# Optimization experiments

Measured on AMD Instinct MI355X. Metric: run time of the kernel, lower is better.

Reference implementation:

```python
import jax, jax.numpy as jnp
import numpy as np

EPS = 1e-5

def _ln(x, s, b):
    mu = jnp.mean(x, axis=-1, keepdims=True)
    var = jnp.mean((x - mu) ** 2, axis=-1, keepdims=True)
    return (x - mu) * jax.lax.rsqrt(var + EPS) * s + b

def _gelu(x):
    return jax.nn.gelu(x, approximate=False)


def setup_inputs() -> dict:
    key = jax.random.key(0)
    ks = jax.random.split(key, 24)
    B, L, C, E, T, FC, MULT = 8, 4096, 128, 1048576, 512, 32, 2
    N = B * L
    inp = {}
    inp['feats'] = jax.random.normal(ks[0], (N, C), jnp.float32)
    inp['edge_index'] = jax.random.randint(ks[1], (2, E), 0, N, jnp.int32)
    inp['edge_attr'] = jax.random.normal(ks[2], (E, 2), jnp.float32) * 0.05  # relative coords
    inp['t'] = jax.random.normal(ks[3], (B, T), jnp.float32)
    inp['norm_vec'] = jnp.ones((N, 1), jnp.float32)
    # LayerNorms
    inp['ln1_scale'] = jnp.ones((C,), jnp.float32); inp['ln1_bias'] = jnp.zeros((C,), jnp.float32)
    inp['ln2_scale'] = jnp.ones((C,), jnp.float32); inp['ln2_bias'] = jnp.zeros((C,), jnp.float32)
    # time mlps: GELU -> Linear(T, 2C)
    sc = lambda k, sh: jax.random.normal(k, sh, jnp.float32) / np.sqrt(sh[0])
    inp['tmlp1_w'] = sc(ks[4], (T, 2 * C)); inp['tmlp1_b'] = jnp.zeros((2 * C,), jnp.float32)
    inp['tmlp2_w'] = sc(ks[5], (T, 2 * C)); inp['tmlp2_b'] = jnp.zeros((2 * C,), jnp.float32)
    # continuous-kernel MLP: 2 -> FC -> FC -> C (depthwise weights)
    inp['ker_w1'] = sc(ks[6], (2, FC)); inp['ker_b1'] = jnp.zeros((FC,), jnp.float32)
    inp['ker_w2'] = sc(ks[7], (FC, FC)); inp['ker_b2'] = jnp.zeros((FC,), jnp.float32)
    inp['ker_w3'] = sc(ks[8], (FC, C)); inp['ker_b3'] = jnp.zeros((C,), jnp.float32)
    inp['conv_bias'] = jnp.zeros((C,), jnp.float32)
    # feedforward mlp: C -> mult*C -> C
    inp['mlp_w1'] = sc(ks[9], (C, MULT * C)); inp['mlp_b1'] = jnp.zeros((MULT * C,), jnp.float32)
    inp['mlp_w2'] = sc(ks[10], (MULT * C, C)); inp['mlp_b2'] = jnp.zeros((C,), jnp.float32)
    return inp


def reference(feats, edge_index, edge_attr, t, norm_vec,
              ln1_scale, ln1_bias, ln2_scale, ln2_bias,
              tmlp1_w, tmlp1_b, tmlp2_w, tmlp2_b,
              ker_w1, ker_b1, ker_w2, ker_b2, ker_w3, ker_b3, conv_bias,
              mlp_w1, mlp_b1, mlp_w2, mlp_b2):
    N, C = feats.shape
    B = t.shape[0]
    q = N // B  # nodes per image

    def modulate(f, ln_s, ln_b, tw, tb):
        h = _ln(f, ln_s, ln_b)
        tm = _gelu(t) @ tw + tb                       # [B, 2C]
        tm = jnp.repeat(tm, q, axis=0)                # [(B q), 2C]
        scale, shift = jnp.split(tm, 2, axis=-1)
        return h * (1.0 + scale) + shift

    # pre-conv modulation
    h = modulate(feats, ln1_scale, ln1_bias, tmlp1_w, tmlp1_b)

    # continuous conv: per-edge depthwise kernel from edge_attr
    k = _gelu(edge_attr @ ker_w1 + ker_b1)
    k = _gelu(k @ ker_w2 + ker_b2)
    w = k @ ker_w3 + ker_b3                           # [E, C]
    src, dst = edge_index[0], edge_index[1]
    msg = w * h[src]                                  # gather + weight  [E, C]
    h = jax.ops.segment_sum(msg, dst, num_segments=N) + conv_bias
    h = h / norm_vec                                  # tg_div normalization

    x = feats + h                                     # residual 1

    # post-conv modulation + MLP
    h2 = modulate(x, ln2_scale, ln2_bias, tmlp2_w, tmlp2_b)
    h2 = _gelu(h2 @ mlp_w1 + mlp_b1) @ mlp_w2 + mlp_b2
    return x + h2                                     # residual 2
```

## Files before the change

### kernel.cpp

```cpp
#include <hip/hip_runtime.h>
#include <hip/hip_bf16.h>

#define C_DIM 128
#define TWO_C 256
#define FC    32
#define T_DIM 512

typedef unsigned int   u32;
typedef unsigned short u16;
typedef unsigned long long u64;
typedef short bf16x8 __attribute__((ext_vector_type(8)));
typedef float f32x4  __attribute__((ext_vector_type(4)));

__device__ __forceinline__ float fast_rcp(float x) {
    return __builtin_amdgcn_rcpf(x);
}
__device__ __forceinline__ float gelu_f(float x) {
    float a = fabsf(x);
    float p = 1.0f + a * (0.19685352f + a * (0.11519450f +
              a * (3.4364302e-4f + a * 0.019527027f)));
    float d  = fast_rcp(p);
    float d2 = d * d;
    float d4 = d2 * d2;
    float s = 0.5f * x;
    return s + s * copysignf(1.0f - d4, x);
}
__device__ __forceinline__ u32 f2bf_bits(float x) {
    u32 u = __float_as_uint(x);
    return (u + 0x7fffu + ((u >> 16) & 1u)) >> 16;
}
__device__ __forceinline__ u32 pack_bf2(float lo, float hi) {
    __hip_bfloat162 p = __float22bfloat162_rn(make_float2(lo, hi));
    u32 r; __builtin_memcpy(&r, &p, 4); return r;
}
__device__ __forceinline__ float bf2f(u16 v) {
    return __uint_as_float((u32)v << 16);
}
__device__ __forceinline__ int hperm(int c) {
    return ((c >> 5) << 5) + ((c & 15) << 1) + ((c >> 4) & 1);
}

__global__ __launch_bounds__(256) void k_tmod(const float* __restrict__ t,
                                              const float* __restrict__ tw1,
                                              const float* __restrict__ tb1,
                                              float* __restrict__ tm1,
                                              const float* __restrict__ tw2,
                                              const float* __restrict__ tb2,
                                              float* __restrict__ tm2) {
    const float* tw = blockIdx.y ? tw2 : tw1;
    const float* tb = blockIdx.y ? tb2 : tb1;
    float*       tm = blockIdx.y ? tm2 : tm1;
    __shared__ float gt[T_DIM];
    int b = blockIdx.x;
    for (int k = threadIdx.x; k < T_DIM; k += 256)
        gt[k] = gelu_f(t[(size_t)b * T_DIM + k]);
    __syncthreads();
    int j = threadIdx.x;
    float acc = tb[j];
    for (int k = 0; k < T_DIM; ++k)
        acc += gt[k] * tw[(size_t)k * TWO_C + j];
    tm[(size_t)b * TWO_C + j] = acc;
}

template <bool BF16OUT, bool ZROW, bool PERM>
__global__ __launch_bounds__(C_DIM) void k_mod(const float* __restrict__ in,
                                               const float* __restrict__ lns,
                                               const float* __restrict__ lnb,
                                               const float* __restrict__ tm,
                                               void* __restrict__ outp, int q, int N) {
    int n = blockIdx.x, c = threadIdx.x;
    if (ZROW && n == N) {
        ((u16*)outp)[(size_t)N * C_DIM + c] = 0;
        return;
    }
    size_t o = (size_t)n * C_DIM + c;
    float v = in[o];
    float s1 = v, s2 = v * v;
#pragma unroll
    for (int off = 32; off > 0; off >>= 1) {
        s1 += __shfl_down(s1, off);
        s2 += __shfl_down(s2, off);
    }
    __shared__ float red[4];
    if ((c & 63) == 0) { red[(c >> 6) * 2] = s1; red[(c >> 6) * 2 + 1] = s2; }
    __syncthreads();
    float mean = (red[0] + red[2]) * (1.0f / C_DIM);
    float ex2  = (red[1] + red[3]) * (1.0f / C_DIM);
    float r    = rsqrtf(ex2 - mean * mean + 1e-5f);
    int b = n / q;
    float scale = tm[(size_t)b * TWO_C + c];
    float shift = tm[(size_t)b * TWO_C + C_DIM + c];
    float h = (v - mean) * r * lns[c] + lnb[c];
    float res = h * (1.0f + scale) + shift;
    if (BF16OUT) {
        int idx = PERM ? hperm(c) : c;
        ((u16*)outp)[(size_t)n * C_DIM + idx] = (u16)f2bf_bits(res);
    } else {
        ((float*)outp)[o] = res;
    }
}

__global__ void k_hist(const int* __restrict__ dst, int* __restrict__ cnt,
                       int* __restrict__ rank, int E) {
    int e = blockIdx.x * 256 + threadIdx.x;
    if (e < E) rank[e] = atomicAdd(&cnt[dst[e]], 1);
}

__global__ __launch_bounds__(1024) void k_scan_bsum(const int* __restrict__ cnt,
                                                    u64* __restrict__ bsum, int N) {
    __shared__ u64 red[1024];
    int t = threadIdx.x;
    int idx = blockIdx.x * 1024 + t;
    int v = (idx < N) ? cnt[idx] : 0;
    red[t] = (u64)(u32)v | ((u64)(u32)((v + 15) >> 4) << 32);
    __syncthreads();
#pragma unroll
    for (int off = 512; off > 0; off >>= 1) {
        if (t < off) red[t] += red[t + off];
        __syncthreads();
    }
    if (t == 0) bsum[blockIdx.x] = red[0];
}

__global__ __launch_bounds__(1024) void k_scan_btop(u64* __restrict__ bsum,
                                                    int* __restrict__ Ttot, int nb) {
    __shared__ u64 tot[1024];
    int t = threadIdx.x;
    u64 v = (t < nb) ? bsum[t] : 0ull;
    tot[t] = v;
    __syncthreads();
    for (int off = 1; off < 1024; off <<= 1) {
        u64 a = (t >= off) ? tot[t - off] : 0ull;
        __syncthreads();
        tot[t] += a;
        __syncthreads();
    }
    if (t < nb) bsum[t] = tot[t] - v;
    if (t == 1023) Ttot[0] = (int)(tot[1023] >> 32);
}

__global__ __launch_bounds__(1024) void k_scan_final(const int* __restrict__ cnt,
                                                     const u64* __restrict__ bsum,
                                                     int* __restrict__ startn,
                                                     int4* __restrict__ tinfo, int N) {
    __shared__ u64 tot[1024];
    int t = threadIdx.x;
    int idx = blockIdx.x * 1024 + t;
    int v = (idx < N) ? cnt[idx] : 0;
    u64 pk = (u64)(u32)v | ((u64)(u32)((v + 15) >> 4) << 32);
    tot[t] = pk;
    __syncthreads();
    for (int off = 1; off < 1024; off <<= 1) {
        u64 a = (t >= off) ? tot[t - off] : 0ull;
        __syncthreads();
        tot[t] += a;
        __syncthreads();
    }
    if (idx >= N) return;
    u64 ex = tot[t] - pk + bsum[blockIdx.x];
    int rd = (int)(ex & 0xffffffffull);
    int rt = (int)(ex >> 32);
    startn[idx] = rd;
    int nt = (v + 15) >> 4;
    int e = rd + v;
    for (int k = 0; k < nt; ++k)
        tinfo[rt + k] = make_int4(idx, rd + 16 * k, e, 0);
}

__global__ void k_sed(const int* __restrict__ ei,
                      const int* __restrict__ rank,
                      const int* __restrict__ startn,
                      const float* __restrict__ ea,
                      uint2* __restrict__ sed2, int E) {
    int e = blockIdx.x * 256 + threadIdx.x;
    if (e >= E) return;
    int pos = startn[ei[E + e]] + rank[e];
    float2 av = ((const float2*)ea)[e];
    uint2 v;
    v.x = pack_bf2(av.x, av.y);
    v.y = (u32)ei[e];
    sed2[pos] = v;
}

__global__ __launch_bounds__(256) void k_edgek2s(
        const uint2* __restrict__ sed2,
        const float* __restrict__ w1, const float* __restrict__ b1,
        const u16* __restrict__ w2kf, const float* __restrict__ b2,
        u32* __restrict__ k2h, int E) {
    int l = threadIdx.x & 63, wv = threadIdx.x >> 6;
    int lr = l & 15, g = l >> 4;
    int wbase = blockIdx.x * 256 + wv * 64;

    bf16x8 wb0 = *(const bf16x8*)(w2kf + (size_t)l * 8);
    bf16x8 wb1 = *(const bf16x8*)(w2kf + (size_t)(64 + l) * 8);
    f32x4 bi0, bi1;
    {
        float v0 = b2[lr], v1 = b2[16 + lr];
        bi0[0] = v0; bi0[1] = v0; bi0[2] = v0; bi0[3] = v0;
        bi1[0] = v1; bi1[1] = v1; bi1[2] = v1; bi1[3] = v1;
    }
    float w1x[8], w1y[8], b1v[8];
#pragma unroll
    for (int j = 0; j < 8; ++j) {
        w1x[j] = w1[8 * g + j];
        w1y[j] = w1[FC + 8 * g + j];
        b1v[j] = b1[8 * g + j];
    }
#pragma unroll
    for (int c = 0; c < 4; ++c) {
        int cb = wbase + 16 * c;
        int pA = cb + lr;
        float ax = 0.f, ay = 0.f;
        if (pA < E) {
            u32 pr = sed2[pA].x;
            ax = bf2f((u16)(pr & 0xffffu));
            ay = bf2f((u16)(pr >> 16));
        }
        union { u32 w[4]; bf16x8 v; } au;
#pragma unroll
        for (int m = 0; m < 4; ++m) {
            float v0 = gelu_f(fmaf(ax, w1x[2 * m],     fmaf(ay, w1y[2 * m],     b1v[2 * m])));
            float v1 = gelu_f(fmaf(ax, w1x[2 * m + 1], fmaf(ay, w1y[2 * m + 1], b1v[2 * m + 1])));
            au.w[m] = pack_bf2(v0, v1);
        }
        f32x4 d0 = __builtin_amdgcn_mfma_f32_16x16x32_bf16(au.v, wb0, bi0, 0, 0, 0);
        f32x4 d1 = __builtin_amdgcn_mfma_f32_16x16x32_bf16(au.v, wb1, bi1, 0, 0, 0);
#pragma unroll
        for (int r = 0; r < 4; ++r) {
            int pD = cb + 4 * g + r;
            if (pD < E) {
                u32 pk = pack_bf2(gelu_f(d0[r]), gelu_f(d1[r]));
                k2h[(size_t)pD * 16 + lr] = pk;
            }
        }
    }
}

#define PREP_TOT (32768 + 32768 + 4096 + 1024)
__global__ __launch_bounds__(256) void k_prep(const float* __restrict__ mw1,
                                              const float* __restrict__ mw2,
                                              const float* __restrict__ kw3,
                                              const float* __restrict__ kw2,
                                              u16* __restrict__ w1f,
                                              u16* __restrict__ w2f,
                                              u16* __restrict__ w3f,
                                              u16* __restrict__ w2kf) {
    int t = blockIdx.x * 256 + threadIdx.x;
    if (t < 32768) {
        int j = t & 7, l = (t >> 3) & 63, f = t >> 9;
        int ks = f & 3, nt = f >> 2;
        int k = ks * 32 + ((l >> 4) << 3) + j, n = nt * 16 + (l & 15);
        w1f[t] = (u16)f2bf_bits(mw1[(size_t)k * TWO_C + n]);
    } else if (t < 65536) {
        int t2 = t - 32768;
        int j = t2 & 7, l = (t2 >> 3) & 63, f = t2 >> 9;
        int ks = f & 7, nt = f >> 3;
        int k = ks * 32 + ((l >> 4) << 3) + j, n = nt * 16 + (l & 15);
        w2f[t2] = (u16)f2bf_bits(mw2[(size_t)k * C_DIM + n]);
    } else if (t < 69632) {
        int t3 = t - 65536;
        int j = t3 & 7, l = (t3 >> 3) & 63, nt = t3 >> 9;
        int kk = ((l >> 4) << 3) + j;
        int k = (kk >> 1) + ((kk & 1) << 4);
        int n = nt * 16 + (l & 15);
        w3f[t3] = (u16)f2bf_bits(kw3[(size_t)k * C_DIM + n]);
    } else if (t < PREP_TOT) {
        int t4 = t - 69632;
        int j = t4 & 7, l = (t4 >> 3) & 63, nt = t4 >> 9;
        int kk = ((l >> 4) << 3) + j;
        int n = nt * 16 + (l & 15);
        w2kf[t4] = (u16)f2bf_bits(kw2[(size_t)kk * FC + n]);
    }
}

__global__ __launch_bounds__(256, 5) void k_conv4(
        const u16* __restrict__ h_mod,
        const int* __restrict__ Ttot,
        const int4* __restrict__ tinfo,
        const u32* __restrict__ k2h,
        const uint2* __restrict__ sed2,
        const u16* __restrict__ w3f, const float* __restrict__ kb3,
        float* __restrict__ xbuf, int N) {
    int l = threadIdx.x & 63, wv = threadIdx.x >> 6;
    int lr = l & 15, g = l >> 4;

    bf16x8 w3b[8];
#pragma unroll
    for (int nt = 0; nt < 8; ++nt)
        w3b[nt] = *(const bf16x8*)(w3f + ((size_t)nt * 64 + l) * 8);
    float b3c[8];
#pragma unroll
    for (int nt = 0; nt < 8; ++nt) b3c[nt] = kb3[nt * 16 + lr];
    const f32x4 zc = {0.f, 0.f, 0.f, 0.f};
    const u32* h32 = (const u32*)h_mod;

    int T = Ttot[0];
    int nw = gridDim.x * 4;
#pragma unroll 1
    for (int t = blockIdx.x * 4 + wv; t < T; t += nw) {
        int4 ti = tinfo[t];
        int n = ti.x, p0 = ti.y, e = ti.z;
        int pa = p0 + lr;
        bf16x8 a = {0, 0, 0, 0, 0, 0, 0, 0};
        if (pa < e) a = *(const bf16x8*)(k2h + (size_t)pa * 16 + g * 4);
        int srcv[4];
#pragma unroll
        for (int r = 0; r < 4; ++r) {
            int pp = p0 + 4 * g + r;
            srcv[r] = (pp < e) ? (int)sed2[pp].y : N;
        }
        const u32* h0p = h32 + (size_t)srcv[0] * 64 + lr;
        const u32* h1p = h32 + (size_t)srcv[1] * 64 + lr;
        const u32* h2p = h32 + (size_t)srcv[2] * 64 + lr;
        const u32* h3p = h32 + (size_t)srcv[3] * 64 + lr;
        float acc[8];
#pragma unroll
        for (int j = 0; j < 4; ++j) {
            f32x4 w0 = __builtin_amdgcn_mfma_f32_16x16x32_bf16(a, w3b[2 * j],     zc, 0, 0, 0);
            f32x4 w1 = __builtin_amdgcn_mfma_f32_16x16x32_bf16(a, w3b[2 * j + 1], zc, 0, 0, 0);
            u32 u0 = h0p[j * 16], u1 = h1p[j * 16], u2 = h2p[j * 16], u3 = h3p[j * 16];
            float l0 = __uint_as_float(u0 << 16), h0 = __uint_as_float(u0 & 0xffff0000u);
            float l1 = __uint_as_float(u1 << 16), h1 = __uint_as_float(u1 & 0xffff0000u);
            float l2 = __uint_as_float(u2 << 16), h2 = __uint_as_float(u2 & 0xffff0000u);
            float l3 = __uint_as_float(u3 << 16), h3 = __uint_as_float(u3 & 0xffff0000u);
            acc[2 * j]     = w0[0] * l0 + w0[1] * l1 + w0[2] * l2 + w0[3] * l3
                           + b3c[2 * j] * (l0 + l1 + l2 + l3);
            acc[2 * j + 1] = w1[0] * h0 + w1[1] * h1 + w1[2] * h2 + w1[3] * h3
                           + b3c[2 * j + 1] * (h0 + h1 + h2 + h3);
        }
#pragma unroll
        for (int nt = 0; nt < 8; ++nt) {
            acc[nt] += __shfl_xor(acc[nt], 16, 64);
            acc[nt] += __shfl_xor(acc[nt], 32, 64);
        }
        float v0 = (g == 0) ? acc[0] : (g == 1) ? acc[2] : (g == 2) ? acc[4] : acc[6];
        float v1 = (g == 0) ? acc[1] : (g == 1) ? acc[3] : (g == 2) ? acc[5] : acc[7];
        float* row = xbuf + (size_t)n * C_DIM + 32 * g + lr;
        atomicAdd(row, v0);
        atomicAdd(row + 16, v1);
    }
}

__global__ __launch_bounds__(C_DIM) void k_post(const float* __restrict__ feats,
                                                const float* __restrict__ xbuf,
                                                const float* __restrict__ cbias,
                                                const float* __restrict__ normv,
                                                const float* __restrict__ tm2,
                                                const float* __restrict__ ln2s,
                                                const float* __restrict__ ln2b,
                                                float* __restrict__ out,
                                                u16* __restrict__ xmb, int q) {
    int n = blockIdx.x, c = threadIdx.x;
    size_t o = (size_t)n * C_DIM + c;
    float v = feats[o] + (xbuf[o] + cbias[c]) * fast_rcp(normv[n]);
    out[o] = v;
    float s1 = v, s2 = v * v;
#pragma unroll
    for (int off = 32; off > 0; off >>= 1) {
        s1 += __shfl_down(s1, off);
        s2 += __shfl_down(s2, off);
    }
    __shared__ float red[4];
    if ((c & 63) == 0) { red[(c >> 6) * 2] = s1; red[(c >> 6) * 2 + 1] = s2; }
    __syncthreads();
    float mean = (red[0] + red[2]) * (1.0f / C_DIM);
    float ex2  = (red[1] + red[3]) * (1.0f / C_DIM);
    float r    = rsqrtf(ex2 - mean * mean + 1e-5f);
    int b = n / q;
    float scale = tm2[(size_t)b * TWO_C + c];
    float shift = tm2[(size_t)b * TWO_C + C_DIM + c];
    float h = (v - mean) * r * ln2s[c] + ln2b[c];
    xmb[o] = (u16)f2bf_bits(h * (1.0f + scale) + shift);
}

__global__ __launch_bounds__(256, 8) void k_ffn2(const u16* __restrict__ xm,
                                                 const u16* __restrict__ w1f,
                                                 const float* __restrict__ b1,
                                                 const u16* __restrict__ w2f,
                                                 const float* __restrict__ b2,
                                                 float* __restrict__ xio, int N) {
    __shared__ u16 sm[4096];
    int tid = threadIdx.x, w = tid >> 6, l = tid & 63;
    int lr = l & 15, g = l >> 4;
    int n0 = blockIdx.x * 16;

    bf16x8 a[4];
    const u16* xrow = xm + (size_t)(n0 + lr) * C_DIM;
#pragma unroll
    for (int ks = 0; ks < 4; ++ks)
        a[ks] = *(const bf16x8*)(xrow + ks * 32 + g * 8);

    f32x4 acc[4];
#pragma unroll
    for (int i = 0; i < 4; ++i) {
        int nt = w + 4 * i;
        float bv = b1[nt * 16 + lr];
        acc[i][0] = bv; acc[i][1] = bv; acc[i][2] = bv; acc[i][3] = bv;
#pragma unroll
        for (int ks = 0; ks < 4; ++ks) {
            bf16x8 bfr = *(const bf16x8*)(w1f + ((size_t)(nt * 4 + ks) * 64 + l) * 8);
            acc[i] = __builtin_amdgcn_mfma_f32_16x16x32_bf16(a[ks], bfr, acc[i], 0, 0, 0);
        }
    }
#pragma unroll
    for (int i = 0; i < 4; ++i) {
        int nt = w + 4 * i;
#pragma unroll
        for (int r = 0; r < 4; ++r) {
            int row = 4 * g + r, col = nt * 16 + lr;
            int byte = row * 512 + ((col * 2) ^ ((row & 7) << 4));
            sm[byte >> 1] = (u16)f2bf_bits(gelu_f(acc[i][r]));
        }
    }
    __syncthreads();
    f32x4 acc2[2];
#pragma unroll
    for (int i = 0; i < 2; ++i) {
        int nt2 = 2 * w + i;
        float bv = b2[nt2 * 16 + lr];
        acc2[i][0] = bv; acc2[i][1] = bv; acc2[i][2] = bv; acc2[i][3] = bv;
    }
#pragma unroll
    for (int ks = 0; ks < 8; ++ks) {
        int byte = lr * 512 + ((ks * 64 + g * 16) ^ ((lr & 7) << 4));
        bf16x8 a2 = *(const bf16x8*)(sm + (byte >> 1));
#pragma unroll
        for (int i = 0; i < 2; ++i) {
            int nt2 = 2 * w + i;
            bf16x8 bfr = *(const bf16x8*)(w2f + ((size_t)(nt2 * 8 + ks) * 64 + l) * 8);
            acc2[i] = __builtin_amdgcn_mfma_f32_16x16x32_bf16(a2, bfr, acc2[i], 0, 0, 0);
        }
    }
#pragma unroll
    for (int i = 0; i < 2; ++i) {
        int nt2 = 2 * w + i;
#pragma unroll
        for (int r = 0; r < 4; ++r) {
            size_t o = (size_t)(n0 + 4 * g + r) * C_DIM + nt2 * 16 + lr;
            xio[o] += acc2[i][r];
        }
    }
}

__global__ __launch_bounds__(256) void k_edge_atomic(
        const int* __restrict__ ei, const float* __restrict__ ea,
        const float* __restrict__ w1, const float* __restrict__ b1,
        const float* __restrict__ w2, const float* __restrict__ b2,
        const float* __restrict__ w3, const float* __restrict__ b3,
        const u16* __restrict__ h_mod, float* __restrict__ xacc, int E) {
    int e = blockIdx.x * 256 + threadIdx.x;
    if (e >= E) return;
    int src = ei[e], dst = ei[E + e];
    float ax = ea[(size_t)e * 2], ay = ea[(size_t)e * 2 + 1];
    float k1[FC];
#pragma unroll
    for (int i = 0; i < FC; ++i) k1[i] = gelu_f(ax * w1[i] + ay * w1[FC + i] + b1[i]);
    float k2v[FC];
#pragma unroll
    for (int j = 0; j < FC; ++j) {
        float acc = b2[j];
#pragma unroll
        for (int i = 0; i < FC; ++i) acc += k1[i] * w2[i * FC + j];
        k2v[j] = gelu_f(acc);
    }
    const u16* hrow = h_mod + (size_t)src * C_DIM;
    float* orow = xacc + (size_t)dst * C_DIM;
    for (int c = 0; c < C_DIM; ++c) {
        float wv = b3[c];
#pragma unroll
        for (int j = 0; j < FC; ++j) wv += k2v[j] * w3[j * C_DIM + c];
        atomicAdd(&orow[c], wv * bf2f(hrow[hperm(c)]));
    }
}

__global__ void k_finish(const float* __restrict__ feats, const float* __restrict__ cbias,
                         const float* __restrict__ normv, float* __restrict__ xbuf, int NC) {
    int i = blockIdx.x * 256 + threadIdx.x;
    if (i >= NC) return;
    int c = i & (C_DIM - 1);
    int n = i >> 7;
    xbuf[i] = feats[i] + (xbuf[i] + cbias[c]) / normv[n];
}

extern "C" void kernel_launch(void* const* d_in, const int* in_sizes, int n_in,
                              void* d_out, int out_size, void* d_ws, size_t ws_size,
                              hipStream_t stream) {
    const float* feats = (const float*)d_in[0];
    const int*   ei    = (const int*)d_in[1];
    const float* ea    = (const float*)d_in[2];
    const float* t     = (const float*)d_in[3];
    const float* normv = (const float*)d_in[4];
    const float* ln1s  = (const float*)d_in[5];
    const float* ln1b  = (const float*)d_in[6];
    const float* ln2s  = (const float*)d_in[7];
    const float* ln2b  = (const float*)d_in[8];
    const float* tw1   = (const float*)d_in[9];
    const float* tb1   = (const float*)d_in[10];
    const float* tw2   = (const float*)d_in[11];
    const float* tb2   = (const float*)d_in[12];
    const float* kw1   = (const float*)d_in[13];
    const float* kb1   = (const float*)d_in[14];
    const float* kw2   = (const float*)d_in[15];
    const float* kb2   = (const float*)d_in[16];
    const float* kw3   = (const float*)d_in[17];
    const float* kb3   = (const float*)d_in[18];
    const float* cbias = (const float*)d_in[19];
    const float* mw1   = (const float*)d_in[20];
    const float* mb1   = (const float*)d_in[21];
    const float* mw2   = (const float*)d_in[22];
    const float* mb2   = (const float*)d_in[23];
    float* out = (float*)d_out;

    const int N = in_sizes[0] / C_DIM;
    const int E = in_sizes[1] / 2;
    const int B = in_sizes[3] / T_DIM;
    const int q = N / B;
    const int nb = (N + 1023) / 1024;

    char* wp = (char*)d_ws;
    auto alloc = [&](size_t bytes) -> char* {
        char* p = wp; wp += (bytes + 255) & ~(size_t)255; return p;
    };
    float* tm1    = (float*)alloc((size_t)B * TWO_C * 4);
    float* tm2    = (float*)alloc((size_t)B * TWO_C * 4);
    u16*   h_mod  = (u16*)alloc(((size_t)N + 1) * C_DIM * 2);
    u16*   xmb    = (u16*)alloc((size_t)N * C_DIM * 2);
    u16*   w1f    = (u16*)alloc((size_t)C_DIM * TWO_C * 2);
    u16*   w2f    = (u16*)alloc((size_t)TWO_C * C_DIM * 2);
    u16*   w3f    = (u16*)alloc((size_t)FC * C_DIM * 2);
    u16*   w2kf   = (u16*)alloc((size_t)FC * FC * 2);
    int*   cnt    = (int*)alloc(((size_t)N + 1) * 4);
    int*   startn = (int*)alloc((size_t)N * 4);
    int*   rank   = (int*)alloc((size_t)E * 4);
    u64*   bsum   = (u64*)alloc(((size_t)nb + 1) * 8);
    int*   Ttot   = (int*)alloc(256);
    int4*  tinfo  = (int4*)alloc(((size_t)E / 16 + N + 64) * 16);
    float* xbuf   = (float*)alloc((size_t)N * C_DIM * 4);
    uint2* sed2   = (uint2*)alloc(((size_t)E + 16) * 8);
    size_t fixed = (size_t)(wp - (char*)d_ws);
    bool can_sort = ws_size >= fixed + ((size_t)E + 16) * 64;
    u32* k2h = (u32*)alloc(((size_t)E + 16) * 64);

    const int eb = (E + 255) / 256;

    k_tmod<<<dim3(B, 2), 256, 0, stream>>>(t, tw1, tb1, tm1, tw2, tb2, tm2);
    k_mod<true, true, true><<<N + 1, C_DIM, 0, stream>>>(feats, ln1s, ln1b, tm1,
                                                         h_mod, q, N);
    k_prep<<<(PREP_TOT + 255) / 256, 256, 0, stream>>>(mw1, mw2, kw3, kw2,
                                                       w1f, w2f, w3f, w2kf);

    if (can_sort) {
        hipMemsetAsync(cnt, 0, ((size_t)N + 1) * 4, stream);
        k_hist<<<eb, 256, 0, stream>>>(ei + E, cnt, rank, E);
        k_scan_bsum<<<nb, 1024, 0, stream>>>(cnt, bsum, N);
        k_scan_btop<<<1, 1024, 0, stream>>>(bsum, Ttot, nb);
        k_scan_final<<<nb, 1024, 0, stream>>>(cnt, bsum, startn, tinfo, N);
        k_sed<<<eb, 256, 0, stream>>>(ei, rank, startn, ea, sed2, E);
        k_edgek2s<<<eb, 256, 0, stream>>>(sed2, kw1, kb1, w2kf, kb2, k2h, E);
        hipMemsetAsync(xbuf, 0, (size_t)N * C_DIM * 4, stream);
        k_conv4<<<3072, 256, 0, stream>>>(h_mod, Ttot, tinfo, k2h, sed2,
                                          w3f, kb3, xbuf, N);
        k_post<<<N, C_DIM, 0, stream>>>(feats, xbuf, cbias, normv, tm2,
                                        ln2s, ln2b, out, xmb, q);
    } else {
        hipMemsetAsync(out, 0, (size_t)N * C_DIM * 4, stream);
        k_edge_atomic<<<eb, 256, 0, stream>>>(ei, ea, kw1, kb1, kw2, kb2, kw3, kb3,
                                              h_mod, out, E);
        int nc = N * C_DIM;
        k_finish<<<(nc + 255) / 256, 256, 0, stream>>>(feats, cbias, normv, out, nc);
        k_mod<true, false, false><<<N, C_DIM, 0, stream>>>(out, ln2s, ln2b, tm2,
                                                           xmb, q, N);
    }

    k_ffn2<<<N / 16, 256, 0, stream>>>(xmb, w1f, mb1, w2f, mb2, out, N);
}
```

Baseline: 227.0 us.

## Fuse edge-kernel MLP first layers into conv kernel via LDS transpose

Removes the separate k_edgek2s pass, which wrote a 64-byte-per-edge bf16 hidden activation buffer that the conv kernel then read back. The conv kernel now computes the first two kernel-MLP layers per 16-edge tile in registers and MFMA, then transposes the result through a swizzled per-wave LDS tile into the A-operand layout. This drops about 128 MB of global traffic and a launch, at the cost of extra ALU and register pressure in the conv kernel. It also lowers the workspace requirement for taking the sorted path.

```diff
diff --git a/kernel.cpp b/kernel.cpp
--- a/kernel.cpp
+++ b/kernel.cpp
@@ -180,60 +180,6 @@
     v.x = pack_bf2(av.x, av.y);
     v.y = (u32)ei[e];
     sed2[pos] = v;
-}
-
-__global__ __launch_bounds__(256) void k_edgek2s(
-        const uint2* __restrict__ sed2,
-        const float* __restrict__ w1, const float* __restrict__ b1,
-        const u16* __restrict__ w2kf, const float* __restrict__ b2,
-        u32* __restrict__ k2h, int E) {
-    int l = threadIdx.x & 63, wv = threadIdx.x >> 6;
-    int lr = l & 15, g = l >> 4;
-    int wbase = blockIdx.x * 256 + wv * 64;
-
-    bf16x8 wb0 = *(const bf16x8*)(w2kf + (size_t)l * 8);
-    bf16x8 wb1 = *(const bf16x8*)(w2kf + (size_t)(64 + l) * 8);
-    f32x4 bi0, bi1;
-    {
-        float v0 = b2[lr], v1 = b2[16 + lr];
-        bi0[0] = v0; bi0[1] = v0; bi0[2] = v0; bi0[3] = v0;
-        bi1[0] = v1; bi1[1] = v1; bi1[2] = v1; bi1[3] = v1;
-    }
-    float w1x[8], w1y[8], b1v[8];
-#pragma unroll
-    for (int j = 0; j < 8; ++j) {
-        w1x[j] = w1[8 * g + j];
-        w1y[j] = w1[FC + 8 * g + j];
-        b1v[j] = b1[8 * g + j];
-    }
-#pragma unroll
-    for (int c = 0; c < 4; ++c) {
-        int cb = wbase + 16 * c;
-        int pA = cb + lr;
-        float ax = 0.f, ay = 0.f;
-        if (pA < E) {
-            u32 pr = sed2[pA].x;
-            ax = bf2f((u16)(pr & 0xffffu));
-            ay = bf2f((u16)(pr >> 16));
-        }
-        union { u32 w[4]; bf16x8 v; } au;
-#pragma unroll
-        for (int m = 0; m < 4; ++m) {
-            float v0 = gelu_f(fmaf(ax, w1x[2 * m],     fmaf(ay, w1y[2 * m],     b1v[2 * m])));
-            float v1 = gelu_f(fmaf(ax, w1x[2 * m + 1], fmaf(ay, w1y[2 * m + 1], b1v[2 * m + 1])));
-            au.w[m] = pack_bf2(v0, v1);
-        }
-        f32x4 d0 = __builtin_amdgcn_mfma_f32_16x16x32_bf16(au.v, wb0, bi0, 0, 0, 0);
-        f32x4 d1 = __builtin_amdgcn_mfma_f32_16x16x32_bf16(au.v, wb1, bi1, 0, 0, 0);
-#pragma unroll
-        for (int r = 0; r < 4; ++r) {
-            int pD = cb + 4 * g + r;
-            if (pD < E) {
-                u32 pk = pack_bf2(gelu_f(d0[r]), gelu_f(d1[r]));
-                k2h[(size_t)pD * 16 + lr] = pk;
-            }
-        }
-    }
 }
 
 #define PREP_TOT (32768 + 32768 + 4096 + 1024)
@@ -277,10 +223,12 @@
         const u16* __restrict__ h_mod,
         const int* __restrict__ Ttot,
         const int4* __restrict__ tinfo,
-        const u32* __restrict__ k2h,
         const uint2* __restrict__ sed2,
-        const u16* __restrict__ w3f, const float* __restrict__ kb3,
+        const float* __restrict__ kw1, const float* __restrict__ kb1,
+        const u16* __restrict__ w2kf, const float* __restrict__ kb2,
+        const u16* __restrict__ w3f,  const float* __restrict__ kb3,
         float* __restrict__ xbuf, int N) {
+    __shared__ u32 lds[4][16][16];
     int l = threadIdx.x & 63, wv = threadIdx.x >> 6;
     int lr = l & 15, g = l >> 4;
 
@@ -288,11 +236,27 @@
 #pragma unroll
     for (int nt = 0; nt < 8; ++nt)
         w3b[nt] = *(const bf16x8*)(w3f + ((size_t)nt * 64 + l) * 8);
+    bf16x8 wb0 = *(const bf16x8*)(w2kf + (size_t)l * 8);
+    bf16x8 wb1 = *(const bf16x8*)(w2kf + (size_t)(64 + l) * 8);
+    f32x4 bi0, bi1;
+    {
+        float v0 = kb2[lr], v1 = kb2[16 + lr];
+        bi0[0] = v0; bi0[1] = v0; bi0[2] = v0; bi0[3] = v0;
+        bi1[0] = v1; bi1[1] = v1; bi1[2] = v1; bi1[3] = v1;
+    }
     float b3c[8];
 #pragma unroll
     for (int nt = 0; nt < 8; ++nt) b3c[nt] = kb3[nt * 16 + lr];
+    float w1x[8], w1y[8], b1v[8];
+#pragma unroll
+    for (int j = 0; j < 8; ++j) {
+        w1x[j] = kw1[8 * g + j];
+        w1y[j] = kw1[FC + 8 * g + j];
+        b1v[j] = kb1[8 * g + j];
+    }
     const f32x4 zc = {0.f, 0.f, 0.f, 0.f};
     const u32* h32 = (const u32*)h_mod;
+    int gg = g ^ ((lr >> 1) & 3);
 
     int T = Ttot[0];
     int nw = gridDim.x * 4;
@@ -301,14 +265,35 @@
         int4 ti = tinfo[t];
         int n = ti.x, p0 = ti.y, e = ti.z;
         int pa = p0 + lr;
-        bf16x8 a = {0, 0, 0, 0, 0, 0, 0, 0};
-        if (pa < e) a = *(const bf16x8*)(k2h + (size_t)pa * 16 + g * 4);
+        float ax = 0.f, ay = 0.f;
+        if (pa < e) {
+            u32 pr = sed2[pa].x;
+            ax = bf2f((u16)(pr & 0xffffu));
+            ay = bf2f((u16)(pr >> 16));
+        }
         int srcv[4];
 #pragma unroll
         for (int r = 0; r < 4; ++r) {
             int pp = p0 + 4 * g + r;
             srcv[r] = (pp < e) ? (int)sed2[pp].y : N;
         }
+        union { u32 w[4]; bf16x8 v; } au;
+#pragma unroll
+        for (int m = 0; m < 4; ++m) {
+            float v0 = gelu_f(fmaf(ax, w1x[2 * m],     fmaf(ay, w1y[2 * m],     b1v[2 * m])));
+            float v1 = gelu_f(fmaf(ax, w1x[2 * m + 1], fmaf(ay, w1y[2 * m + 1], b1v[2 * m + 1])));
+            au.w[m] = pack_bf2(v0, v1);
+        }
+        f32x4 d0 = __builtin_amdgcn_mfma_f32_16x16x32_bf16(au.v, wb0, bi0, 0, 0, 0);
+        f32x4 d1 = __builtin_amdgcn_mfma_f32_16x16x32_bf16(au.v, wb1, bi1, 0, 0, 0);
+#pragma unroll
+        for (int r = 0; r < 4; ++r) {
+            int row = 4 * g + r;
+            u32 pk = pack_bf2(gelu_f(d0[r]), gelu_f(d1[r]));
+            lds[wv][row][lr ^ (((row >> 1) & 3) << 2)] = pk;
+        }
+        __builtin_amdgcn_s_waitcnt(0xc07f);
+        bf16x8 a = *(const bf16x8*)&lds[wv][lr][4 * gg];
         const u32* h0p = h32 + (size_t)srcv[0] * 64 + lr;
         const u32* h1p = h32 + (size_t)srcv[1] * 64 + lr;
         const u32* h2p = h32 + (size_t)srcv[2] * 64 + lr;
@@ -536,10 +521,9 @@
     int*   Ttot   = (int*)alloc(256);
     int4*  tinfo  = (int4*)alloc(((size_t)E / 16 + N + 64) * 16);
     float* xbuf   = (float*)alloc((size_t)N * C_DIM * 4);
+    size_t fixed = (size_t)(wp - (char*)d_ws);
+    bool can_sort = ws_size >= fixed + ((size_t)E + 16) * 8;
     uint2* sed2   = (uint2*)alloc(((size_t)E + 16) * 8);
-    size_t fixed = (size_t)(wp - (char*)d_ws);
-    bool can_sort = ws_size >= fixed + ((size_t)E + 16) * 64;
-    u32* k2h = (u32*)alloc(((size_t)E + 16) * 64);
 
     const int eb = (E + 255) / 256;
 
@@ -556,10 +540,10 @@
         k_scan_btop<<<1, 1024, 0, stream>>>(bsum, Ttot, nb);
         k_scan_final<<<nb, 1024, 0, stream>>>(cnt, bsum, startn, tinfo, N);
         k_sed<<<eb, 256, 0, stream>>>(ei, rank, startn, ea, sed2, E);
-        k_edgek2s<<<eb, 256, 0, stream>>>(sed2, kw1, kb1, w2kf, kb2, k2h, E);
         hipMemsetAsync(xbuf, 0, (size_t)N * C_DIM * 4, stream);
-        k_conv4<<<3072, 256, 0, stream>>>(h_mod, Ttot, tinfo, k2h, sed2,
-                                          w3f, kb3, xbuf, N);
+        k_conv4<<<3072, 256, 0, stream>>>(h_mod, Ttot, tinfo, sed2,
+                                          kw1, kb1, w2kf, kb2, w3f, kb3,
+                                          xbuf, N);
         k_post<<<N, C_DIM, 0, stream>>>(feats, xbuf, cbias, normv, tm2,
                                         ln2s, ln2b, out, xmb, q);
     } else {
```

Result: slower. 309.2 us (+36.3%).

## Fuse post-conv residual, LayerNorm and modulation into the FFN kernel

Applied to the files above, without the earlier changes.

Folds the per-node post-conv step (residual add, normalisation, second LayerNorm and time modulation) into the MFMA feed-forward kernel. Each block now builds its 16-row modulated bf16 tile and fp32 residual in LDS, so the separate k_post launch and the xmb round trip through global memory go away, along with the read-modify-write of out. The cost is a serial 8-iteration prologue with two barriers per row pair, plus more LDS per block, which may lower occupancy.

```diff
diff --git a/kernel.cpp b/kernel.cpp
--- a/kernel.cpp
+++ b/kernel.cpp
@@ -341,55 +341,68 @@
     }
 }
 
-__global__ __launch_bounds__(C_DIM) void k_post(const float* __restrict__ feats,
-                                                const float* __restrict__ xbuf,
-                                                const float* __restrict__ cbias,
-                                                const float* __restrict__ normv,
-                                                const float* __restrict__ tm2,
-                                                const float* __restrict__ ln2s,
-                                                const float* __restrict__ ln2b,
-                                                float* __restrict__ out,
-                                                u16* __restrict__ xmb, int q) {
-    int n = blockIdx.x, c = threadIdx.x;
-    size_t o = (size_t)n * C_DIM + c;
-    float v = feats[o] + (xbuf[o] + cbias[c]) * fast_rcp(normv[n]);
-    out[o] = v;
-    float s1 = v, s2 = v * v;
-#pragma unroll
-    for (int off = 32; off > 0; off >>= 1) {
-        s1 += __shfl_down(s1, off);
-        s2 += __shfl_down(s2, off);
-    }
-    __shared__ float red[4];
-    if ((c & 63) == 0) { red[(c >> 6) * 2] = s1; red[(c >> 6) * 2 + 1] = s2; }
-    __syncthreads();
-    float mean = (red[0] + red[2]) * (1.0f / C_DIM);
-    float ex2  = (red[1] + red[3]) * (1.0f / C_DIM);
-    float r    = rsqrtf(ex2 - mean * mean + 1e-5f);
-    int b = n / q;
-    float scale = tm2[(size_t)b * TWO_C + c];
-    float shift = tm2[(size_t)b * TWO_C + C_DIM + c];
-    float h = (v - mean) * r * ln2s[c] + ln2b[c];
-    xmb[o] = (u16)f2bf_bits(h * (1.0f + scale) + shift);
-}
-
-__global__ __launch_bounds__(256, 8) void k_ffn2(const u16* __restrict__ xm,
-                                                 const u16* __restrict__ w1f,
-                                                 const float* __restrict__ b1,
-                                                 const u16* __restrict__ w2f,
-                                                 const float* __restrict__ b2,
-                                                 float* __restrict__ xio, int N) {
+__global__ __launch_bounds__(256) void k_ffn3(const float* __restrict__ feats,
+                                              const float* __restrict__ xbuf,
+                                              const float* __restrict__ cbias,
+                                              const float* __restrict__ normv,
+                                              const float* __restrict__ tm2,
+                                              const float* __restrict__ ln2s,
+                                              const float* __restrict__ ln2b,
+                                              const u16* __restrict__ w1f,
+                                              const float* __restrict__ b1,
+                                              const u16* __restrict__ w2f,
+                                              const float* __restrict__ b2,
+                                              float* __restrict__ out, int q) {
+    __shared__ u16 xmt[2048];
+    __shared__ float xt[16][128];
     __shared__ u16 sm[4096];
-    int tid = threadIdx.x, w = tid >> 6, l = tid & 63;
+    __shared__ float red2[2][4];
+    int tid = threadIdx.x;
+    int n0 = blockIdx.x * 16;
+
+    {
+        int gi = tid >> 7, c = tid & 127;
+#pragma unroll 1
+        for (int it = 0; it < 8; ++it) {
+            int rA = 2 * it + gi;
+            int n = n0 + rA;
+            size_t o = (size_t)n * C_DIM + c;
+            float v = feats[o] + (xbuf[o] + cbias[c]) * fast_rcp(normv[n]);
+            float s1 = v, s2 = v * v;
+#pragma unroll
+            for (int off = 32; off > 0; off >>= 1) {
+                s1 += __shfl_down(s1, off);
+                s2 += __shfl_down(s2, off);
+            }
+            if ((c & 63) == 0) {
+                red2[gi][(c >> 6) * 2] = s1;
+                red2[gi][(c >> 6) * 2 + 1] = s2;
+            }
+            __syncthreads();
+            float mean = (red2[gi][0] + red2[gi][2]) * (1.0f / C_DIM);
+            float ex2  = (red2[gi][1] + red2[gi][3]) * (1.0f / C_DIM);
+            float r    = rsqrtf(ex2 - mean * mean + 1e-5f);
+            int b = n / q;
+            float scale = tm2[(size_t)b * TWO_C + c];
+            float shift = tm2[(size_t)b * TWO_C + C_DIM + c];
+            float h = (v - mean) * r * ln2s[c] + ln2b[c];
+            float res = h * (1.0f + scale) + shift;
+            int byte = rA * 256 + ((c * 2) ^ ((rA & 7) << 4));
+            xmt[byte >> 1] = (u16)f2bf_bits(res);
+            xt[rA][c] = v;
+            __syncthreads();
+        }
+    }
+
+    int w = tid >> 6, l = tid & 63;
     int lr = l & 15, g = l >> 4;
-    int n0 = blockIdx.x * 16;
 
     bf16x8 a[4];
-    const u16* xrow = xm + (size_t)(n0 + lr) * C_DIM;
-#pragma unroll
-    for (int ks = 0; ks < 4; ++ks)
-        a[ks] = *(const bf16x8*)(xrow + ks * 32 + g * 8);
-
+#pragma unroll
+    for (int ks = 0; ks < 4; ++ks) {
+        int byte = lr * 256 + ((ks * 64 + g * 16) ^ ((lr & 7) << 4));
+        a[ks] = *(const bf16x8*)((const char*)xmt + byte);
+    }
     f32x4 acc[4];
 #pragma unroll
     for (int i = 0; i < 4; ++i) {
@@ -437,7 +450,7 @@
 #pragma unroll
         for (int r = 0; r < 4; ++r) {
             size_t o = (size_t)(n0 + 4 * g + r) * C_DIM + nt2 * 16 + lr;
-            xio[o] += acc2[i][r];
+            out[o] = xt[4 * g + r][nt2 * 16 + lr] + acc2[i][r];
         }
     }
 }
@@ -471,15 +484,6 @@
         for (int j = 0; j < FC; ++j) wv += k2v[j] * w3[j * C_DIM + c];
         atomicAdd(&orow[c], wv * bf2f(hrow[hperm(c)]));
     }
-}
-
-__global__ void k_finish(const float* __restrict__ feats, const float* __restrict__ cbias,
-                         const float* __restrict__ normv, float* __restrict__ xbuf, int NC) {
-    int i = blockIdx.x * 256 + threadIdx.x;
-    if (i >= NC) return;
-    int c = i & (C_DIM - 1);
-    int n = i >> 7;
-    xbuf[i] = feats[i] + (xbuf[i] + cbias[c]) / normv[n];
 }
 
 extern "C" void kernel_launch(void* const* d_in, const int* in_sizes, int n_in,
@@ -524,7 +528,6 @@
     float* tm1    = (float*)alloc((size_t)B * TWO_C * 4);
     float* tm2    = (float*)alloc((size_t)B * TWO_C * 4);
     u16*   h_mod  = (u16*)alloc(((size_t)N + 1) * C_DIM * 2);
-    u16*   xmb    = (u16*)alloc((size_t)N * C_DIM * 2);
     u16*   w1f    = (u16*)alloc((size_t)C_DIM * TWO_C * 2);
     u16*   w2f    = (u16*)alloc((size_t)TWO_C * C_DIM * 2);
     u16*   w3f    = (u16*)alloc((size_t)FC * C_DIM * 2);
@@ -548,6 +551,7 @@
                                                          h_mod, q, N);
     k_prep<<<(PREP_TOT + 255) / 256, 256, 0, stream>>>(mw1, mw2, kw3, kw2,
                                                        w1f, w2f, w3f, w2kf);
+    hipMemsetAsync(xbuf, 0, (size_t)N * C_DIM * 4, stream);
 
     if (can_sort) {
         hipMemsetAsync(cnt, 0, ((size_t)N + 1) * 4, stream);
@@ -557,20 +561,13 @@
         k_scan_final<<<nb, 1024, 0, stream>>>(cnt, bsum, startn, tinfo, N);
         k_sed<<<eb, 256, 0, stream>>>(ei, rank, startn, ea, sed2, E);
         k_edgek2s<<<eb, 256, 0, stream>>>(sed2, kw1, kb1, w2kf, kb2, k2h, E);
-        hipMemsetAsync(xbuf, 0, (size_t)N * C_DIM * 4, stream);
         k_conv4<<<3072, 256, 0, stream>>>(h_mod, Ttot, tinfo, k2h, sed2,
                                           w3f, kb3, xbuf, N);
-        k_post<<<N, C_DIM, 0, stream>>>(feats, xbuf, cbias, normv, tm2,
-                                        ln2s, ln2b, out, xmb, q);
     } else {
-        hipMemsetAsync(out, 0, (size_t)N * C_DIM * 4, stream);
         k_edge_atomic<<<eb, 256, 0, stream>>>(ei, ea, kw1, kb1, kw2, kb2, kw3, kb3,
-                                              h_mod, out, E);
-        int nc = N * C_DIM;
-        k_finish<<<(nc + 255) / 256, 256, 0, stream>>>(feats, cbias, normv, out, nc);
-        k_mod<true, false, false><<<N, C_DIM, 0, stream>>>(out, ln2s, ln2b, tm2,
-                                                           xmb, q, N);
-    }
-
-    k_ffn2<<<N / 16, 256, 0, stream>>>(xmb, w1f, mb1, w2f, mb2, out, N);
-}
+                                              h_mod, xbuf, E);
+    }
+
+    k_ffn3<<<N / 16, 256, 0, stream>>>(feats, xbuf, cbias, normv, tm2, ln2s, ln2b,
+                                       w1f, mb1, w2f, mb2, out, q);
+}
```

Measured after the change: 223.9 us. About the same (-1.4%).
